# Kernel optimization log

Hardware: AMD Instinct MI355X
Metric: run time of the kernel (lower is better)

Reference implementation:

```python
import jax, jax.numpy as jnp
import numpy as np

S = 2048  # expert group size
M = 768   # hidden size
H = 3072  # intermediate size
E = 16    # num experts


def top2_gating(gates):
    # gates: [G, S, E]
    G, S_, E_ = gates.shape
    C = 2 * S_ // E_
    mask_dtype = jnp.int32
    index_1 = jnp.argmax(gates, axis=-1)
    mask_1 = jax.nn.one_hot(index_1, E_, dtype=mask_dtype)
    gate_1 = jnp.einsum('GSE,GSE->GS', gates, mask_1)
    gates_without_top_1 = gates * (1 - mask_1)
    index_2 = jnp.argmax(gates_without_top_1, axis=-1)
    mask_2 = jax.nn.one_hot(index_2, E_, dtype=mask_dtype)
    gate_2 = jnp.einsum('GSE,GSE->GS', gates_without_top_1, mask_2)
    pos_1 = jnp.cumsum(mask_1, axis=-2) - mask_1
    mask_1 = mask_1 * (pos_1 < C)
    pos_1 = jnp.einsum('GSE,GSE->GS', pos_1, mask_1)
    mask_1_count = jnp.sum(mask_1, axis=-2)
    mask_1_flat = jnp.sum(mask_1, axis=-1)
    pos_2 = jnp.cumsum(mask_2, axis=-2) - mask_2 + jnp.expand_dims(mask_1_count, -2)
    mask_2 = mask_2 * (pos_2 < C)
    pos_2 = jnp.einsum('GSE,GSE->GS', pos_2, mask_2)
    mask_2_flat = jnp.sum(mask_2, axis=-1)
    gate_1 = gate_1 * mask_1_flat
    gate_2 = gate_2 * mask_2_flat
    denom = gate_1 + gate_2
    denom = jnp.where(denom > 0, denom, jnp.ones_like(denom))
    gate_1 = gate_1 / denom
    gate_2 = gate_2 / denom
    a = jnp.expand_dims(gate_1 * mask_1_flat, -1) * jax.nn.one_hot(index_1, E_, dtype=gates.dtype)
    b = jax.nn.one_hot(pos_1, C, dtype=gates.dtype)
    first = jnp.einsum('GSE,GSC->GSEC', a, b)
    a = jnp.expand_dims(gate_2 * mask_2_flat, -1) * jax.nn.one_hot(index_2, E_, dtype=gates.dtype)
    b = jax.nn.one_hot(pos_2, C, dtype=gates.dtype)
    second = jnp.einsum('GSE,GSC->GSEC', a, b)
    combined_tensor = first + second
    dispatch_tensor = combined_tensor.astype(jnp.bool_)
    return combined_tensor, dispatch_tensor


def setup_inputs() -> dict:
    key = jax.random.key(0)
    k1, k2, k3, k4 = jax.random.split(key, 4)
    inputs = jax.random.normal(k1, (4, 1024, M), dtype=jnp.float32)
    wg = jax.random.normal(k2, (M, E), dtype=jnp.float32) * (1.0 / np.sqrt(M))
    wi = jax.random.normal(k3, (E, M, H), dtype=jnp.float32) * (1.0 / np.sqrt(M))
    wo = jax.random.normal(k4, (E, H, M), dtype=jnp.float32) * (1.0 / np.sqrt(H))
    return {"inputs": inputs, "wg": wg, "wi": wi, "wo": wo}


def reference(inputs, wg, wi, wo):
    x = jnp.reshape(inputs, (-1, S, M))                      # [G, S, M]
    gates = jax.nn.softmax(jnp.einsum('GSM,ME->GSE', x, wg))
    combined_weights, dispatch_mask = top2_gating(gates)
    dispatched = jnp.einsum('GSEC,GSM->EGCM',
                            dispatch_mask.astype(x.dtype), x)
    h = jnp.einsum('EGCM,EMH->EGCH', dispatched, wi)
    h = jax.nn.relu(h)
    expert_out = jnp.einsum('EGCH,EHM->GECM', h, wo)
    out = jnp.einsum('GSEC,GECM->GSM', combined_weights, expert_out)
    return jnp.reshape(out, inputs.shape)
```

## Files before the change

### kernel.cpp

```cpp
#include <hip/hip_runtime.h>
#include <hip/hip_bf16.h>
#include <cstdint>
#include <cstddef>

#define S_TOK 2048
#define M_DIM 768
#define H_DIM 3072
#define E_NUM 16
#define CAP   256

using s16x8 = __attribute__((ext_vector_type(8))) short;
using f32x4 = __attribute__((ext_vector_type(4))) float;

__device__ __forceinline__ unsigned short f2bf(float f) {
    unsigned u = __float_as_uint(f);
    unsigned r = 0x7fffu + ((u >> 16) & 1u);
    return (unsigned short)((u + r) >> 16);
}

__device__ __forceinline__ void async16(const void* g, void* l) {
    __builtin_amdgcn_global_load_lds((const __attribute__((address_space(1))) void*)g,
                                     (__attribute__((address_space(3))) void*)l, 16, 0, 0);
}

__global__ void gating_kernel(const float* __restrict__ x, const float* __restrict__ wg,
                              int* __restrict__ e1o, int* __restrict__ e2o,
                              float* __restrict__ g1o, float* __restrict__ g2o, int ntok) {
    int gid  = blockIdx.x * blockDim.x + threadIdx.x;
    int tok  = gid >> 6;
    int lane = threadIdx.x & 63;
    if (tok >= ntok) return;
    const float* xr = x + (size_t)tok * M_DIM;
    float acc[E_NUM];
#pragma unroll
    for (int e = 0; e < E_NUM; ++e) acc[e] = 0.f;
    for (int m = lane; m < M_DIM; m += 64) {
        float xv = xr[m];
        const float* wr = wg + (size_t)m * E_NUM;
#pragma unroll
        for (int e = 0; e < E_NUM; ++e) acc[e] += xv * wr[e];
    }
#pragma unroll
    for (int off = 32; off >= 1; off >>= 1) {
#pragma unroll
        for (int e = 0; e < E_NUM; ++e) acc[e] += __shfl_xor(acc[e], off, 64);
    }
    if (lane == 0) {
        float mx = acc[0];
#pragma unroll
        for (int e = 1; e < E_NUM; ++e) mx = fmaxf(mx, acc[e]);
        float p[E_NUM]; float s = 0.f;
#pragma unroll
        for (int e = 0; e < E_NUM; ++e) { p[e] = expf(acc[e] - mx); s += p[e]; }
        float inv = 1.f / s;
        int b1 = 0; float v1 = -1.f;
#pragma unroll
        for (int e = 0; e < E_NUM; ++e) { if (p[e] > v1) { v1 = p[e]; b1 = e; } }
        int b2 = 0; float v2 = -1.f;
#pragma unroll
        for (int e = 0; e < E_NUM; ++e) { if (e != b1 && p[e] > v2) { v2 = p[e]; b2 = e; } }
        e1o[tok] = b1; e2o[tok] = b2;
        g1o[tok] = v1 * inv; g2o[tok] = v2 * inv;
    }
}

__global__ void assign_kernel(const int* __restrict__ e1a, const int* __restrict__ e2a,
                              const float* __restrict__ g1a, const float* __restrict__ g2a,
                              int* __restrict__ slot1, int* __restrict__ slot2,
                              float* __restrict__ w1, float* __restrict__ w2,
                              int* __restrict__ tfs, int G) {
    int g    = blockIdx.x;
    int tid  = threadIdx.x;
    int w    = tid >> 6;
    int lane = tid & 63;
    __shared__ int cnt1s[E_NUM];

    for (int i = tid; i < E_NUM * CAP; i += 1024) tfs[(size_t)g * E_NUM * CAP + i] = -1;
    __syncthreads();

    {
        int cnt = 0;
        for (int base = 0; base < S_TOK; base += 64) {
            int t = g * S_TOK + base + lane;
            bool pred = (e1a[t] == w);
            unsigned long long bal = __ballot(pred);
            int prefix = __popcll(bal & ((1ull << lane) - 1ull));
            if (pred) {
                int pos = cnt + prefix;
                if (pos < CAP) {
                    slot1[t] = w * CAP + pos;
                    tfs[((size_t)g * E_NUM + w) * CAP + pos] = base + lane;
                } else {
                    slot1[t] = -1;
                }
            }
            cnt += __popcll(bal);
        }
        if (lane == 0) cnt1s[w] = cnt < CAP ? cnt : CAP;
    }
    __syncthreads();
    {
        int cnt = cnt1s[w];
        for (int base = 0; base < S_TOK; base += 64) {
            int t = g * S_TOK + base + lane;
            bool pred = (e2a[t] == w);
            unsigned long long bal = __ballot(pred);
            int prefix = __popcll(bal & ((1ull << lane) - 1ull));
            if (pred) {
                int pos = cnt + prefix;
                if (pos < CAP) {
                    slot2[t] = w * CAP + pos;
                    tfs[((size_t)g * E_NUM + w) * CAP + pos] = base + lane;
                } else {
                    slot2[t] = -1;
                }
            }
            cnt += __popcll(bal);
        }
    }
    __syncthreads();
    for (int t = tid; t < S_TOK; t += 1024) {
        int gt = g * S_TOK + t;
        float a = slot1[gt] >= 0 ? g1a[gt] : 0.f;
        float b = slot2[gt] >= 0 ? g2a[gt] : 0.f;
        float denom = a + b;
        if (!(denom > 0.f)) denom = 1.f;
        w1[gt] = a / denom;
        w2[gt] = b / denom;
    }
}

__global__ void convert_x_kernel(const float* __restrict__ x, unsigned short* __restrict__ xb,
                                 int ntok) {
    int i4 = blockIdx.x * blockDim.x + threadIdx.x;
    size_t base = (size_t)i4 * 4;
    size_t n_real = (size_t)ntok * M_DIM;
    size_t n_tot  = (size_t)(ntok + 1) * M_DIM;
    if (base >= n_tot) return;
    ushort4 o;
    if (base < n_real) {
        float4 v = *(const float4*)&x[base];
        o.x = f2bf(v.x); o.y = f2bf(v.y); o.z = f2bf(v.z); o.w = f2bf(v.w);
    } else {
        o.x = o.y = o.z = o.w = 0;
    }
    *(ushort4*)&xb[base] = o;
}

__global__ __launch_bounds__(256) void transpose_conv_kernel(const float* __restrict__ src,
                                                             unsigned short* __restrict__ dst,
                                                             int R, int C) {
    __shared__ float T[64][65];
    int e  = blockIdx.z;
    int c0 = blockIdx.x * 64;
    int r0 = blockIdx.y * 64;
    int tid = threadIdx.x;
    int lx = tid & 63, ly = tid >> 6;
    const float* Sp = src + (size_t)e * R * C;
#pragma unroll
    for (int i = 0; i < 16; ++i) {
        int r = i * 4 + ly;
        T[r][lx] = Sp[(size_t)(r0 + r) * C + c0 + lx];
    }
    __syncthreads();
    unsigned short* D = dst + (size_t)e * C * R;
    int rb = (tid & 15) * 4;
    int cy = tid >> 4;
#pragma unroll
    for (int p = 0; p < 4; ++p) {
        int c = p * 16 + cy;
        ushort4 o;
        o.x = f2bf(T[rb + 0][c]);
        o.y = f2bf(T[rb + 1][c]);
        o.z = f2bf(T[rb + 2][c]);
        o.w = f2bf(T[rb + 3][c]);
        *(ushort4*)&D[(size_t)(c0 + c) * R + r0 + rb] = o;
    }
}

template<int KLOOP, bool GATHER>
__global__ __launch_bounds__(256) void mfma_gemm_kernel(
        const unsigned short* __restrict__ A,
        const unsigned short* __restrict__ B,
        const int* __restrict__ tfs,
        void* __restrict__ Out0, void* __restrict__ Out1,
        int G, int N_total, int kstride, int NKH) {
    __shared__ unsigned short As[2][128 * 32];
    __shared__ unsigned short Bs[2][128 * 32];
    __shared__ int rowtok[128];

    int NB  = gridDim.x;
    int bid = blockIdx.x;
    int per = NB >> 3;
    int lid = (bid & 7) * per + (bid >> 3);

    int NT_N = N_total >> 7;
    int c  = lid & 1;
    int r1 = lid >> 1;
    int g  = r1 % G;
    int r2 = r1 / G;
    int n  = r2 % NT_N;
    int r3 = r2 / NT_N;
    int kh = r3 % NKH;
    int e  = r3 / NKH;
    int z  = e * G + g;
    int n0 = n * 128;
    int c0 = c * 128;
    int koff = kh * KLOOP;
    int tid = threadIdx.x;

    if (GATHER) {
        if (tid < 128) rowtok[tid] = tfs[((size_t)g * E_NUM + e) * CAP + c0 + tid];
        __syncthreads();
    }

    int r4 = tid >> 2, l4 = tid & 3;
    const unsigned short *apt0, *apt1;
    if (GATHER) {
        int t0 = rowtok[r4], t1 = rowtok[64 + r4];
        size_t row0 = (t0 < 0) ? (size_t)(G * S_TOK) : (size_t)(g * S_TOK + t0);
        size_t row1 = (t1 < 0) ? (size_t)(G * S_TOK) : (size_t)(g * S_TOK + t1);
        apt0 = A + row0 * kstride + koff + l4 * 8;
        apt1 = A + row1 * kstride + koff + l4 * 8;
    } else {
        apt0 = A + ((size_t)z * CAP + c0 + r4) * kstride + koff + l4 * 8;
        apt1 = apt0 + (size_t)64 * kstride;
    }
    const unsigned short* Bexp = B + (size_t)e * N_total * kstride;
    const unsigned short* bpt0 = Bexp + ((size_t)n0 + r4) * kstride + koff + l4 * 8;
    const unsigned short* bpt1 = bpt0 + (size_t)64 * kstride;

    int wv = tid >> 6;
    int lane = tid & 63;
    int r = lane & 15, q = lane >> 4;
    int wm = wv & 1, wn = wv >> 1;

    f32x4 acc[4][4];
#pragma unroll
    for (int i = 0; i < 4; ++i)
#pragma unroll
        for (int j = 0; j < 4; ++j) acc[i][j] = (f32x4)(0.f);

#define STAGE(b) do {                                    \
        async16(apt0, &As[b][(wv * 16) * 32]);           \
        async16(apt1, &As[b][(64 + wv * 16) * 32]);      \
        async16(bpt0, &Bs[b][(wv * 16) * 32]);           \
        async16(bpt1, &Bs[b][(64 + wv * 16) * 32]);      \
        apt0 += 32; apt1 += 32; bpt0 += 32; bpt1 += 32;  \
    } while (0)

    const int NT = KLOOP / 32;
    STAGE(0);
    __syncthreads();
    int cur = 0;
    for (int t = 0; t < NT; ++t) {
        if (t + 1 < NT) STAGE(cur ^ 1);
        s16x8 af[4], bfr[4];
#pragma unroll
        for (int i = 0; i < 4; ++i)
            af[i] = *(const s16x8*)&As[cur][(wm * 64 + i * 16 + r) * 32 + q * 8];
#pragma unroll
        for (int j = 0; j < 4; ++j)
            bfr[j] = *(const s16x8*)&Bs[cur][(wn * 64 + j * 16 + r) * 32 + q * 8];
#pragma unroll
        for (int i = 0; i < 4; ++i)
#pragma unroll
            for (int j = 0; j < 4; ++j)
                acc[i][j] = __builtin_amdgcn_mfma_f32_16x16x32_bf16(af[i], bfr[j], acc[i][j], 0, 0, 0);
        __syncthreads();
        cur ^= 1;
    }
#undef STAGE

    if (GATHER) {
        unsigned short* H = (unsigned short*)Out0;
#pragma unroll
        for (int i = 0; i < 4; ++i) {
#pragma unroll
            for (int v = 0; v < 4; ++v) {
                int m_loc = wm * 64 + i * 16 + q * 4 + v;
                unsigned short* row = H + ((size_t)z * CAP + c0 + m_loc) * N_total + n0;
#pragma unroll
                for (int j = 0; j < 4; ++j) {
                    int n_loc = wn * 64 + j * 16 + r;
                    row[n_loc] = f2bf(fmaxf(acc[i][j][v], 0.f));
                }
            }
        }
    } else {
        float* O = (float*)(kh ? Out1 : Out0);
#pragma unroll
        for (int i = 0; i < 4; ++i) {
#pragma unroll
            for (int v = 0; v < 4; ++v) {
                int m_loc = wm * 64 + i * 16 + q * 4 + v;
                float* row = O + (((size_t)g * E_NUM + e) * CAP + c0 + m_loc) * N_total + n0;
#pragma unroll
                for (int j = 0; j < 4; ++j) {
                    int n_loc = wn * 64 + j * 16 + r;
                    row[n_loc] = acc[i][j][v];
                }
            }
        }
    }
}

__global__ void combine_kernel(const float* __restrict__ eoA, const float* __restrict__ eoB,
                               const int* __restrict__ slot1, const int* __restrict__ slot2,
                               const float* __restrict__ w1, const float* __restrict__ w2,
                               float* __restrict__ out, int G) {
    int t = blockIdx.x;
    int g = t / S_TOK;
    int tid = threadIdx.x;
    int s1 = slot1[t], s2 = slot2[t];
    float a = w1[t], b = w2[t];
    size_t gb = (size_t)g * E_NUM * CAP * M_DIM;
    const float* p1A = eoA + gb + (size_t)(s1 < 0 ? 0 : s1) * M_DIM;
    const float* p1B = eoB + gb + (size_t)(s1 < 0 ? 0 : s1) * M_DIM;
    const float* p2A = eoA + gb + (size_t)(s2 < 0 ? 0 : s2) * M_DIM;
    const float* p2B = eoB + gb + (size_t)(s2 < 0 ? 0 : s2) * M_DIM;
    for (int m = tid; m < M_DIM; m += 256) {
        float v = 0.f;
        if (s1 >= 0) v += a * (p1A[m] + p1B[m]);
        if (s2 >= 0) v += b * (p2A[m] + p2B[m]);
        out[(size_t)t * M_DIM + m] = v;
    }
}

extern "C" void kernel_launch(void* const* d_in, const int* in_sizes, int n_in,
                              void* d_out, int out_size, void* d_ws, size_t ws_size,
                              hipStream_t stream) {
    const float* x  = (const float*)d_in[0];
    const float* wg = (const float*)d_in[1];
    const float* wi = (const float*)d_in[2];
    const float* wo = (const float*)d_in[3];
    float* out = (float*)d_out;

    int ntok = in_sizes[0] / M_DIM;
    int G = ntok / S_TOK;

    char* wsp = (char*)d_ws;
    auto carve = [&](size_t bytes) {
        void* p = (void*)wsp;
        wsp += (bytes + 255) & ~(size_t)255;
        return p;
    };
    int*   e1    = (int*)carve((size_t)ntok * 4);
    int*   e2    = (int*)carve((size_t)ntok * 4);
    float* g1    = (float*)carve((size_t)ntok * 4);
    float* g2    = (float*)carve((size_t)ntok * 4);
    int*   slot1 = (int*)carve((size_t)ntok * 4);
    int*   slot2 = (int*)carve((size_t)ntok * 4);
    float* w1    = (float*)carve((size_t)ntok * 4);
    float* w2    = (float*)carve((size_t)ntok * 4);
    int*   tfs   = (int*)carve((size_t)G * E_NUM * CAP * 4);
    unsigned short* xb  = (unsigned short*)carve((size_t)(ntok + 1) * M_DIM * 2);
    unsigned short* wiT = (unsigned short*)carve((size_t)E_NUM * H_DIM * M_DIM * 2);
    unsigned short* woT = (unsigned short*)carve((size_t)E_NUM * M_DIM * H_DIM * 2);
    unsigned short* h   = (unsigned short*)carve((size_t)E_NUM * G * CAP * H_DIM * 2);
    float* eo = (float*)carve((size_t)G * E_NUM * CAP * M_DIM * 4);
    float* eoB = (float*)wiT;

    gating_kernel<<<(ntok * 64 + 255) / 256, 256, 0, stream>>>(x, wg, e1, e2, g1, g2, ntok);
    assign_kernel<<<G, 1024, 0, stream>>>(e1, e2, g1, g2, slot1, slot2, w1, w2, tfs, G);

    int nx4 = ((ntok + 1) * M_DIM) / 4;
    convert_x_kernel<<<(nx4 + 255) / 256, 256, 0, stream>>>(x, xb, ntok);
    transpose_conv_kernel<<<dim3(H_DIM / 64, M_DIM / 64, E_NUM), 256, 0, stream>>>(wi, wiT, M_DIM, H_DIM);
    transpose_conv_kernel<<<dim3(M_DIM / 64, H_DIM / 64, E_NUM), 256, 0, stream>>>(wo, woT, H_DIM, M_DIM);

    mfma_gemm_kernel<M_DIM, true><<<(H_DIM / 128) * (CAP / 128) * E_NUM * G, 256, 0, stream>>>(
        xb, wiT, tfs, h, h, G, H_DIM, M_DIM, 1);
    mfma_gemm_kernel<H_DIM / 2, false><<<(M_DIM / 128) * (CAP / 128) * E_NUM * G * 2, 256, 0, stream>>>(
        h, woT, tfs, eo, eoB, G, M_DIM, H_DIM, 2);

    combine_kernel<<<ntok, 256, 0, stream>>>(eo, eoB, slot1, slot2, w1, w2, out, G);
}
```

Measured before the change: 535.5 us.

## Enlarge GEMM tiles to 256 rows, fuse x conversion into gating, merge transposes

The expert GEMM kernel now uses 512-thread blocks covering all 256 capacity rows against a 128-column tile. Each wave computes a 128x32 sub-tile, and the two half-blocks along capacity are gone, so each B tile is loaded once per expert group instead of twice. The bf16 conversion of x, including the zero padding row, moves into the gating kernel, and the wi and wo transposes run in a single launch. This removes two kernel launches and redundant weight traffic, at the cost of more LDS A-fragment reads per MFMA and fewer, larger blocks.

```diff
diff --git a/kernel.cpp b/kernel.cpp
--- a/kernel.cpp
+++ b/kernel.cpp
@@ -25,17 +25,24 @@
 
 __global__ void gating_kernel(const float* __restrict__ x, const float* __restrict__ wg,
                               int* __restrict__ e1o, int* __restrict__ e2o,
-                              float* __restrict__ g1o, float* __restrict__ g2o, int ntok) {
+                              float* __restrict__ g1o, float* __restrict__ g2o,
+                              unsigned short* __restrict__ xb, int ntok) {
     int gid  = blockIdx.x * blockDim.x + threadIdx.x;
     int tok  = gid >> 6;
     int lane = threadIdx.x & 63;
-    if (tok >= ntok) return;
+    if (tok > ntok) return;
+    unsigned short* xbr = xb + (size_t)tok * M_DIM;
+    if (tok == ntok) {
+        for (int m = lane; m < M_DIM; m += 64) xbr[m] = 0;
+        return;
+    }
     const float* xr = x + (size_t)tok * M_DIM;
     float acc[E_NUM];
 #pragma unroll
     for (int e = 0; e < E_NUM; ++e) acc[e] = 0.f;
     for (int m = lane; m < M_DIM; m += 64) {
         float xv = xr[m];
+        xbr[m] = f2bf(xv);
         const float* wr = wg + (size_t)m * E_NUM;
 #pragma unroll
         for (int e = 0; e < E_NUM; ++e) acc[e] += xv * wr[e];
@@ -130,30 +137,28 @@
     }
 }
 
-__global__ void convert_x_kernel(const float* __restrict__ x, unsigned short* __restrict__ xb,
-                                 int ntok) {
-    int i4 = blockIdx.x * blockDim.x + threadIdx.x;
-    size_t base = (size_t)i4 * 4;
-    size_t n_real = (size_t)ntok * M_DIM;
-    size_t n_tot  = (size_t)(ntok + 1) * M_DIM;
-    if (base >= n_tot) return;
-    ushort4 o;
-    if (base < n_real) {
-        float4 v = *(const float4*)&x[base];
-        o.x = f2bf(v.x); o.y = f2bf(v.y); o.z = f2bf(v.z); o.w = f2bf(v.w);
+#define NB_WI ((H_DIM / 64) * (M_DIM / 64) * E_NUM)
+__global__ __launch_bounds__(256) void transpose_conv_kernel(const float* __restrict__ wi,
+                                                             unsigned short* __restrict__ wiT,
+                                                             const float* __restrict__ wo,
+                                                             unsigned short* __restrict__ woT) {
+    __shared__ float T[64][65];
+    int bid = blockIdx.x;
+    const float* src; unsigned short* dst; int R, C, cx, ry, e;
+    if (bid < NB_WI) {
+        int per = (H_DIM / 64) * (M_DIM / 64);
+        e = bid / per; int rem = bid % per;
+        cx = rem % (H_DIM / 64); ry = rem / (H_DIM / 64);
+        R = M_DIM; C = H_DIM; src = wi; dst = wiT;
     } else {
-        o.x = o.y = o.z = o.w = 0;
-    }
-    *(ushort4*)&xb[base] = o;
-}
-
-__global__ __launch_bounds__(256) void transpose_conv_kernel(const float* __restrict__ src,
-                                                             unsigned short* __restrict__ dst,
-                                                             int R, int C) {
-    __shared__ float T[64][65];
-    int e  = blockIdx.z;
-    int c0 = blockIdx.x * 64;
-    int r0 = blockIdx.y * 64;
+        int b2 = bid - NB_WI;
+        int per = (M_DIM / 64) * (H_DIM / 64);
+        e = b2 / per; int rem = b2 % per;
+        cx = rem % (M_DIM / 64); ry = rem / (M_DIM / 64);
+        R = H_DIM; C = M_DIM; src = wo; dst = woT;
+    }
+    int c0 = cx * 64;
+    int r0 = ry * 64;
     int tid = threadIdx.x;
     int lx = tid & 63, ly = tid >> 6;
     const float* Sp = src + (size_t)e * R * C;
@@ -179,15 +184,15 @@
 }
 
 template<int KLOOP, bool GATHER>
-__global__ __launch_bounds__(256) void mfma_gemm_kernel(
+__global__ __launch_bounds__(512, 4) void mfma_gemm_kernel(
         const unsigned short* __restrict__ A,
         const unsigned short* __restrict__ B,
         const int* __restrict__ tfs,
         void* __restrict__ Out0, void* __restrict__ Out1,
         int G, int N_total, int kstride, int NKH) {
-    __shared__ unsigned short As[2][128 * 32];
+    __shared__ unsigned short As[2][256 * 32];
     __shared__ unsigned short Bs[2][128 * 32];
-    __shared__ int rowtok[128];
+    __shared__ int rowtok[256];
 
     int NB  = gridDim.x;
     int bid = blockIdx.x;
@@ -195,58 +200,53 @@
     int lid = (bid & 7) * per + (bid >> 3);
 
     int NT_N = N_total >> 7;
-    int c  = lid & 1;
-    int r1 = lid >> 1;
-    int g  = r1 % G;
-    int r2 = r1 / G;
-    int n  = r2 % NT_N;
-    int r3 = r2 / NT_N;
-    int kh = r3 % NKH;
-    int e  = r3 / NKH;
+    int g  = lid % G;
+    int r1 = lid / G;
+    int n  = r1 % NT_N;
+    int r2 = r1 / NT_N;
+    int kh = r2 % NKH;
+    int e  = r2 / NKH;
     int z  = e * G + g;
     int n0 = n * 128;
-    int c0 = c * 128;
     int koff = kh * KLOOP;
     int tid = threadIdx.x;
 
     if (GATHER) {
-        if (tid < 128) rowtok[tid] = tfs[((size_t)g * E_NUM + e) * CAP + c0 + tid];
+        if (tid < 256) rowtok[tid] = tfs[((size_t)g * E_NUM + e) * CAP + tid];
         __syncthreads();
     }
 
-    int r4 = tid >> 2, l4 = tid & 3;
-    const unsigned short *apt0, *apt1;
+    int r8 = tid >> 2, l4 = tid & 3;
+    const unsigned short *apt0, *apt1, *bpt0;
     if (GATHER) {
-        int t0 = rowtok[r4], t1 = rowtok[64 + r4];
+        int t0 = rowtok[r8], t1 = rowtok[128 + r8];
         size_t row0 = (t0 < 0) ? (size_t)(G * S_TOK) : (size_t)(g * S_TOK + t0);
         size_t row1 = (t1 < 0) ? (size_t)(G * S_TOK) : (size_t)(g * S_TOK + t1);
         apt0 = A + row0 * kstride + koff + l4 * 8;
         apt1 = A + row1 * kstride + koff + l4 * 8;
     } else {
-        apt0 = A + ((size_t)z * CAP + c0 + r4) * kstride + koff + l4 * 8;
-        apt1 = apt0 + (size_t)64 * kstride;
-    }
-    const unsigned short* Bexp = B + (size_t)e * N_total * kstride;
-    const unsigned short* bpt0 = Bexp + ((size_t)n0 + r4) * kstride + koff + l4 * 8;
-    const unsigned short* bpt1 = bpt0 + (size_t)64 * kstride;
+        apt0 = A + ((size_t)z * CAP + r8) * kstride + koff + l4 * 8;
+        apt1 = apt0 + (size_t)128 * kstride;
+    }
+    bpt0 = B + ((size_t)e * N_total + n0 + r8) * kstride + koff + l4 * 8;
 
     int wv = tid >> 6;
     int lane = tid & 63;
     int r = lane & 15, q = lane >> 4;
     int wm = wv & 1, wn = wv >> 1;
 
-    f32x4 acc[4][4];
-#pragma unroll
-    for (int i = 0; i < 4; ++i)
-#pragma unroll
-        for (int j = 0; j < 4; ++j) acc[i][j] = (f32x4)(0.f);
-
-#define STAGE(b) do {                                    \
-        async16(apt0, &As[b][(wv * 16) * 32]);           \
-        async16(apt1, &As[b][(64 + wv * 16) * 32]);      \
-        async16(bpt0, &Bs[b][(wv * 16) * 32]);           \
-        async16(bpt1, &Bs[b][(64 + wv * 16) * 32]);      \
-        apt0 += 32; apt1 += 32; bpt0 += 32; bpt1 += 32;  \
+    f32x4 acc[8][2];
+#pragma unroll
+    for (int i = 0; i < 8; ++i) {
+        acc[i][0] = (f32x4)(0.f);
+        acc[i][1] = (f32x4)(0.f);
+    }
+
+#define STAGE(b) do {                                      \
+        async16(apt0, &As[b][(wv * 16) * 32]);             \
+        async16(apt1, &As[b][(128 + wv * 16) * 32]);       \
+        async16(bpt0, &Bs[b][(wv * 16) * 32]);             \
+        apt0 += 32; apt1 += 32; bpt0 += 32;                \
     } while (0)
 
     const int NT = KLOOP / 32;
@@ -255,18 +255,14 @@
     int cur = 0;
     for (int t = 0; t < NT; ++t) {
         if (t + 1 < NT) STAGE(cur ^ 1);
-        s16x8 af[4], bfr[4];
-#pragma unroll
-        for (int i = 0; i < 4; ++i)
-            af[i] = *(const s16x8*)&As[cur][(wm * 64 + i * 16 + r) * 32 + q * 8];
-#pragma unroll
-        for (int j = 0; j < 4; ++j)
-            bfr[j] = *(const s16x8*)&Bs[cur][(wn * 64 + j * 16 + r) * 32 + q * 8];
-#pragma unroll
-        for (int i = 0; i < 4; ++i)
-#pragma unroll
-            for (int j = 0; j < 4; ++j)
-                acc[i][j] = __builtin_amdgcn_mfma_f32_16x16x32_bf16(af[i], bfr[j], acc[i][j], 0, 0, 0);
+        s16x8 bfr0 = *(const s16x8*)&Bs[cur][(wn * 32 + r) * 32 + q * 8];
+        s16x8 bfr1 = *(const s16x8*)&Bs[cur][(wn * 32 + 16 + r) * 32 + q * 8];
+#pragma unroll
+        for (int i = 0; i < 8; ++i) {
+            s16x8 af = *(const s16x8*)&As[cur][(wm * 128 + i * 16 + r) * 32 + q * 8];
+            acc[i][0] = __builtin_amdgcn_mfma_f32_16x16x32_bf16(af, bfr0, acc[i][0], 0, 0, 0);
+            acc[i][1] = __builtin_amdgcn_mfma_f32_16x16x32_bf16(af, bfr1, acc[i][1], 0, 0, 0);
+        }
         __syncthreads();
         cur ^= 1;
     }
@@ -275,30 +271,28 @@
     if (GATHER) {
         unsigned short* H = (unsigned short*)Out0;
 #pragma unroll
-        for (int i = 0; i < 4; ++i) {
+        for (int i = 0; i < 8; ++i) {
 #pragma unroll
             for (int v = 0; v < 4; ++v) {
-                int m_loc = wm * 64 + i * 16 + q * 4 + v;
-                unsigned short* row = H + ((size_t)z * CAP + c0 + m_loc) * N_total + n0;
-#pragma unroll
-                for (int j = 0; j < 4; ++j) {
-                    int n_loc = wn * 64 + j * 16 + r;
-                    row[n_loc] = f2bf(fmaxf(acc[i][j][v], 0.f));
+                int m_loc = wm * 128 + i * 16 + q * 4 + v;
+                unsigned short* row = H + ((size_t)z * CAP + m_loc) * N_total + n0 + wn * 32;
+#pragma unroll
+                for (int j = 0; j < 2; ++j) {
+                    row[j * 16 + r] = f2bf(fmaxf(acc[i][j][v], 0.f));
                 }
             }
         }
     } else {
         float* O = (float*)(kh ? Out1 : Out0);
 #pragma unroll
-        for (int i = 0; i < 4; ++i) {
+        for (int i = 0; i < 8; ++i) {
 #pragma unroll
             for (int v = 0; v < 4; ++v) {
-                int m_loc = wm * 64 + i * 16 + q * 4 + v;
-                float* row = O + (((size_t)g * E_NUM + e) * CAP + c0 + m_loc) * N_total + n0;
-#pragma unroll
-                for (int j = 0; j < 4; ++j) {
-                    int n_loc = wn * 64 + j * 16 + r;
-                    row[n_loc] = acc[i][j][v];
+                int m_loc = wm * 128 + i * 16 + q * 4 + v;
+                float* row = O + (((size_t)g * E_NUM + e) * CAP + m_loc) * N_total + n0 + wn * 32;
+#pragma unroll
+                for (int j = 0; j < 2; ++j) {
+                    row[j * 16 + r] = acc[i][j][v];
                 }
             }
         }
@@ -361,17 +355,14 @@
     float* eo = (float*)carve((size_t)G * E_NUM * CAP * M_DIM * 4);
     float* eoB = (float*)wiT;
 
-    gating_kernel<<<(ntok * 64 + 255) / 256, 256, 0, stream>>>(x, wg, e1, e2, g1, g2, ntok);
+    gating_kernel<<<((ntok + 1) * 64 + 255) / 256, 256, 0, stream>>>(
+        x, wg, e1, e2, g1, g2, xb, ntok);
     assign_kernel<<<G, 1024, 0, stream>>>(e1, e2, g1, g2, slot1, slot2, w1, w2, tfs, G);
-
-    int nx4 = ((ntok + 1) * M_DIM) / 4;
-    convert_x_kernel<<<(nx4 + 255) / 256, 256, 0, stream>>>(x, xb, ntok);
-    transpose_conv_kernel<<<dim3(H_DIM / 64, M_DIM / 64, E_NUM), 256, 0, stream>>>(wi, wiT, M_DIM, H_DIM);
-    transpose_conv_kernel<<<dim3(M_DIM / 64, H_DIM / 64, E_NUM), 256, 0, stream>>>(wo, woT, H_DIM, M_DIM);
-
-    mfma_gemm_kernel<M_DIM, true><<<(H_DIM / 128) * (CAP / 128) * E_NUM * G, 256, 0, stream>>>(
+    transpose_conv_kernel<<<2 * NB_WI, 256, 0, stream>>>(wi, wiT, wo, woT);
+
+    mfma_gemm_kernel<M_DIM, true><<<(H_DIM / 128) * E_NUM * G, 512, 0, stream>>>(
         xb, wiT, tfs, h, h, G, H_DIM, M_DIM, 1);
-    mfma_gemm_kernel<H_DIM / 2, false><<<(M_DIM / 128) * (CAP / 128) * E_NUM * G * 2, 256, 0, stream>>>(
+    mfma_gemm_kernel<H_DIM / 2, false><<<(M_DIM / 128) * E_NUM * G * 2, 512, 0, stream>>>(
         h, woT, tfs, eo, eoB, G, M_DIM, H_DIM, 2);
 
     combine_kernel<<<ntok, 256, 0, stream>>>(eo, eoB, slot1, slot2, w1, w2, out, G);
```

Measured after the change: 534.4 us. About the same (-0.2%).
